# Optimization experiments

Hardware: AMD Instinct MI355X
Metric: run time of the kernel (lower is better)

The kernel has to match this reference:

```python
import jax, jax.numpy as jnp
import numpy as np
from jax import lax

COCO_80_TO_91 = [1,2,3,4,5,6,7,8,9,10,11,13,14,15,16,17,18,19,20,21,22,23,24,25,27,28,31,32,33,34,35,36,37,38,39,40,41,42,43,44,46,47,48,49,50,51,52,53,54,55,56,57,58,59,60,61,62,63,64,65,67,70,72,73,74,75,76,77,78,79,80,81,82,84,85,86,87,88,89,90]

CONF = 0.25      # self.confidence
IOU_THR = 0.7    # ultralytics NMS default
TOPK = 1000      # candidate cap before NMS
MAX_DET = 300    # ultralytics max_det default
MAX_WH = 7680.0  # per-class offset trick
IMG_SZ = 640.0   # yolov8 letterboxed input size


def setup_inputs() -> dict:
    key = jax.random.key(0)
    preds = jax.random.uniform(key, (32, 84, 8400), dtype=jnp.float32)
    return {"preds": preds}


def _nms_single(boxes, scores):
    """Greedy NMS on score-descending boxes [K,4] (class-offset xyxy). Returns keep mask [K]."""
    K = boxes.shape[0]
    area = (boxes[:, 2] - boxes[:, 0]) * (boxes[:, 3] - boxes[:, 1])  # [K]
    lt = jnp.maximum(boxes[:, None, :2], boxes[None, :, :2])          # [K,K,2]
    rb = jnp.minimum(boxes[:, None, 2:], boxes[None, :, 2:])
    wh = jnp.clip(rb - lt, 0.0)
    inter = wh[..., 0] * wh[..., 1]
    iou = inter / (area[:, None] + area[None, :] - inter + 1e-7)       # [K,K]
    idx = jnp.arange(K)
    sup = (iou > IOU_THR) & (idx[None, :] > idx[:, None])              # i suppresses later j

    def body(i, keep):
        return jnp.where(keep[i], keep & ~sup[i], keep)

    return lax.fori_loop(0, K, body, jnp.ones((K,), dtype=bool))


def reference(preds):
    # preds: [B, 84, N] -> [B, N, 84]
    p = jnp.transpose(preds, (0, 2, 1))
    box_xywh = p[..., :4] * IMG_SZ           # xywh in pixels on 640x640 canvas
    cls = p[..., 4:]                          # [B, N, 80]
    scores = jnp.max(cls, axis=-1)            # best-class confidence
    labels = jnp.argmax(cls, axis=-1)         # 0..79
    xy, wh = box_xywh[..., :2], box_xywh[..., 2:]
    xyxy = jnp.concatenate([xy - wh * 0.5, xy + wh * 0.5], axis=-1)  # decode

    # confidence filter + top-K candidate selection (score-descending)
    s_masked = jnp.where(scores > CONF, scores, -1.0)
    top_s, top_i = lax.top_k(s_masked, TOPK)                          # [B,TOPK]
    top_b = jnp.take_along_axis(xyxy, top_i[..., None], axis=1)      # [B,TOPK,4]
    top_l = jnp.take_along_axis(labels, top_i, axis=1)               # [B,TOPK]

    # per-class NMS via class offset
    off_b = top_b + (top_l.astype(top_b.dtype) * MAX_WH)[..., None]
    keep = jax.vmap(_nms_single)(off_b, top_s) & (top_s > CONF)

    # select final max_det detections, zero-pad invalid slots
    fin_s = jnp.where(keep, top_s, -1.0)
    out_s, out_i = lax.top_k(fin_s, MAX_DET)                          # [B,MAX_DET]
    out_b = jnp.take_along_axis(top_b, out_i[..., None], axis=1)
    out_l = jnp.take_along_axis(top_l, out_i, axis=1)
    valid = out_s > CONF
    boxes = jnp.where(valid[..., None], out_b, 0.0)
    scores_out = jnp.where(valid, out_s, 0.0)
    mapped = jnp.asarray(COCO_80_TO_91, dtype=jnp.int64)[out_l]       # COCO 80 -> 91 ids
    labels_out = jnp.where(valid, mapped, 0)
    return boxes, scores_out, labels_out
```

## Files before the change

### kernel.cpp

```cpp
#include <hip/hip_runtime.h>
#include <stdint.h>

typedef unsigned long long u64;
typedef unsigned int u32;

#define BATCH 32
#define NCH 84
#define NA 8400
#define NCLS 80
#define TOPK 1000
#define MAXDET 300
#define CONF 0.25f
#define IOU_T 0.7f
#define MAX_WH 7680.0f
#define IMG_SZ 640.0f
#define NT 1024
#define KPT 9
#define NCOPY 8
#define HPAD 260

__device__ __constant__ float coco_map_f[NCLS] = {
    1,2,3,4,5,6,7,8,9,10,11,13,14,15,16,17,18,19,20,21,22,23,24,25,27,28,
    31,32,33,34,35,36,37,38,39,40,41,42,43,44,46,47,48,49,50,51,52,53,54,
    55,56,57,58,59,60,61,62,63,64,65,67,70,72,73,74,75,76,77,78,79,80,81,
    82,84,85,86,87,88,89,90};

__device__ inline u64 shflx64(u64 v, int m) {
    int lo = __shfl_xor((int)(u32)(v & 0xFFFFFFFFull), m, 64);
    int hi = __shfl_xor((int)(u32)(v >> 32), m, 64);
    return ((u64)(u32)hi << 32) | (u32)lo;
}

__global__ __launch_bounds__(256)
void decode_kernel(const float* __restrict__ preds,
                   u64* __restrict__ keys,
                   float4* __restrict__ boxes,
                   int* __restrict__ labels) {
    const int QPB = NA / 4;
    int gid = blockIdx.x * 256 + threadIdx.x;
    if (gid >= BATCH * QPB) return;
    int b = gid / QPB;
    int q = gid - b * QPB;
    int a0 = q * 4;
    const float* p = preds + (size_t)b * NCH * NA + a0;

    float4 x = *(const float4*)(p);
    float4 y = *(const float4*)(p + NA);
    float4 w = *(const float4*)(p + 2 * NA);
    float4 h = *(const float4*)(p + 3 * NA);

    float4 best = *(const float4*)(p + 4 * NA);
    int lx = 0, ly = 0, lz = 0, lw = 0;
#pragma unroll 16
    for (int c = 1; c < NCLS; ++c) {
        const float4 v = *(const float4*)(p + (size_t)(4 + c) * NA);
        lx = (v.x > best.x) ? c : lx;  best.x = fmaxf(v.x, best.x);
        ly = (v.y > best.y) ? c : ly;  best.y = fmaxf(v.y, best.y);
        lz = (v.z > best.z) ? c : lz;  best.z = fmaxf(v.z, best.z);
        lw = (v.w > best.w) ? c : lw;  best.w = fmaxf(v.w, best.w);
    }

    float bs[4] = {best.x, best.y, best.z, best.w};
    int   bl[4] = {lx, ly, lz, lw};
    float cx[4] = {x.x, x.y, x.z, x.w};
    float cy[4] = {y.x, y.y, y.z, y.w};
    float cw[4] = {w.x, w.y, w.z, w.w};
    float ch[4] = {h.x, h.y, h.z, h.w};

    u64* kp = keys + (size_t)b * NA + a0;
    float4* bp = boxes + (size_t)b * NA + a0;
    int* lp = labels + (size_t)b * NA + a0;

#pragma unroll
    for (int i = 0; i < 4; ++i) {
        float fx = cx[i] * IMG_SZ, fy = cy[i] * IMG_SZ;
        float fw = cw[i] * IMG_SZ, fh = ch[i] * IMG_SZ;
        float hw = fw * 0.5f, hh = fh * 0.5f;
        bp[i] = make_float4(fx - hw, fy - hh, fx + hw, fy + hh);
        float s = (bs[i] > CONF) ? bs[i] : -1.0f;
        u32 fb = __float_as_uint(s);
        u32 u = (fb & 0x80000000u) ? ~fb : (fb | 0x80000000u);
        kp[i] = ((u64)u << 14) | (u64)(16383 - (a0 + i));
    }
    *(int4*)lp = make_int4(bl[0], bl[1], bl[2], bl[3]);
}

__global__ __launch_bounds__(NT)
void select_nms_kernel(const u64* __restrict__ keys,
                       const float4* __restrict__ boxes,
                       const int* __restrict__ labels,
                       float* __restrict__ out) {
    const int b = blockIdx.x;
    const int t = threadIdx.x;
    const int lane = t & 63, wid = t >> 6;

    __shared__ u64 skey[NT];
    __shared__ float offb[TOPK][4];
    __shared__ float area_s[TOPK];
    __shared__ unsigned char lb8[TOPK];
    __shared__ unsigned char keep[TOPK];
    __shared__ u64 cmask2[NCLS][16];
    __shared__ unsigned short rows[NCLS][64];
    __shared__ int sh_hist[NCOPY * HPAD];
    __shared__ int selB, selK, hselS, cnt, nselS, ktot_s;
    __shared__ int wsum[16], woff[16];

    u64 kreg[KPT];
    const u64* kb = keys + (size_t)b * NA;
    int nk = 0;
    for (int i = t; i < NA; i += NT) kreg[nk++] = kb[i];

    u64 P = 0ull;
    int kk = TOPK;
    int nsel = 0;
    for (int d = 5; d >= 0; --d) {
        for (int i = t; i < NCOPY * HPAD; i += NT) sh_hist[i] = 0;
        __syncthreads();
        u64 hmask = (~0ull) << (8 * (d + 1));
        int* myh = sh_hist + (wid & (NCOPY - 1)) * HPAD;
        for (int i = 0; i < KPT; ++i) {
            if (i < nk) {
                u64 key = kreg[i];
                if (((key ^ P) & hmask) == 0ull)
                    atomicAdd(&myh[(int)((key >> (8 * d)) & 255)], 1);
            }
        }
        __syncthreads();
        if (t < 64) {
            int h0 = 0, h1 = 0, h2 = 0, h3 = 0;
            for (int c = 0; c < NCOPY; ++c) {
                const int* hp = sh_hist + c * HPAD + 4 * t;
                h0 += hp[0]; h1 += hp[1]; h2 += hp[2]; h3 += hp[3];
            }
            int s = h0 + h1 + h2 + h3;
            int S = s;
            #pragma unroll
            for (int off = 1; off < 64; off <<= 1) {
                int o = __shfl_down(S, off, 64);
                if (t + off < 64) S += o;
            }
            int Snext = S - s;
            int c3 = Snext + h3, c2 = c3 + h2, c1 = c2 + h1, c0 = c1 + h0;
            int cand = -1, above = 0;
            if (c0 >= kk) {
                if      (c3 >= kk) { cand = 4 * t + 3; above = Snext; }
                else if (c2 >= kk) { cand = 4 * t + 2; above = c3; }
                else if (c1 >= kk) { cand = 4 * t + 1; above = c2; }
                else               { cand = 4 * t;     above = c1; }
            }
            int pc = (cand < 0) ? 0 : (((cand + 1) << 16) | (kk - above));
            #pragma unroll
            for (int off = 32; off; off >>= 1)
                pc = max(pc, __shfl_down(pc, off, 64));
            pc = __shfl(pc, 0, 64);
            int B = (pc >> 16) - 1;
            if (t == (B >> 2)) {
                int m4 = B & 3;
                selB = B;
                selK = pc & 0xFFFF;
                hselS = (m4 == 0) ? h0 : (m4 == 1) ? h1 : (m4 == 2) ? h2 : h3;
            }
        }
        __syncthreads();
        P |= ((u64)selB) << (8 * d);
        kk = selK;
        nsel = TOPK - kk + hselS;
        if (nsel <= NT) break;
        __syncthreads();
    }

    if (t == 0) cnt = 0;
    __syncthreads();
    for (int i = 0; i < KPT; ++i) {
        bool p = (i < nk) && (kreg[i] >= P);
        u64 m = __ballot(p);
        int base = 0;
        if (lane == 0) base = atomicAdd(&cnt, (int)__popcll(m));
        base = __shfl(base, 0, 64);
        if (p) skey[base + (int)__popcll(m & ((1ull << lane) - 1ull))] = kreg[i];
    }
    if (t < NT - nsel) skey[nsel + t] = 0ull;
    __syncthreads();

    u64 myk = skey[t];
    for (int size = 2; size <= NT; size <<= 1) {
        bool up = ((t & size) == 0);
        for (int stride = size >> 1; stride; stride >>= 1) {
            u64 pk;
            if (stride >= 64) {
                __syncthreads(); skey[t] = myk; __syncthreads();
                pk = skey[t ^ stride];
            } else {
                pk = shflx64(myk, stride);
            }
            bool tlow = ((t & stride) == 0);
            u64 mn = (myk < pk) ? myk : pk;
            u64 mx = (myk < pk) ? pk : myk;
            myk = up ? (tlow ? mx : mn) : (tlow ? mn : mx);
        }
    }

    for (int i = t; i < NCLS * 16; i += NT) ((u64*)cmask2)[i] = 0ull;
    __syncthreads();

    int my_a = -1, my_L = 0;
    if (t < TOPK) {
        my_a = 16383 - (int)(myk & 16383ull);
        my_L = labels[(size_t)b * NA + my_a];
        lb8[t] = (unsigned char)my_L;
        float4 bx = boxes[(size_t)b * NA + my_a];
        float off = (float)my_L * MAX_WH;
        float ox0 = bx.x + off, oy0 = bx.y + off, ox1 = bx.z + off, oy1 = bx.w + off;
        offb[t][0] = ox0; offb[t][1] = oy0; offb[t][2] = ox1; offb[t][3] = oy1;
        area_s[t] = (ox1 - ox0) * (oy1 - oy0);
        keep[t] = 1;
        atomicOr(&cmask2[my_L][t >> 6], 1ull << (t & 63));
    }
    __syncthreads();

    for (int c = wid; c < NCLS; c += 16) {
        u64 w = (lane < 16) ? cmask2[c][lane] : 0ull;
        int cw = __popcll(w);
        int pre = cw;
        #pragma unroll
        for (int off = 1; off < 16; off <<= 1) {
            int o = __shfl_up(pre, off, 64);
            if (lane >= off) pre += o;
        }
        int n = __shfl(pre, 15, 64);
        pre -= cw;
        if (n == 0) continue;
        if (n <= 64) {
            if (lane < 16) {
                u64 ww = w; int base = pre, boff = lane << 6;
                while (ww) {
                    int bit = __ffsll((long long)ww) - 1;
                    ww &= ww - 1;
                    rows[c][base++] = (unsigned short)(boff + bit);
                }
            }
            int j = (lane < n) ? (int)rows[c][lane] : (int)rows[c][0];
            float x0 = offb[j][0], y0 = offb[j][1];
            float x1 = offb[j][2], y1 = offb[j][3];
            float ar = area_s[j];
            u64 colm = 0ull;
            for (int i = 0; i < n; ++i) {
                float hx0 = __shfl(x0, i, 64);
                float hy0 = __shfl(y0, i, 64);
                float hx1 = __shfl(x1, i, 64);
                float hy1 = __shfl(y1, i, 64);
                float ha  = __shfl(ar, i, 64);
                float lx = fmaxf(hx0, x0), ly = fmaxf(hy0, y0);
                float rx = fminf(hx1, x1), ry = fminf(hy1, y1);
                float ww2 = fmaxf(rx - lx, 0.0f);
                float hh2 = fmaxf(ry - ly, 0.0f);
                float inter = ww2 * hh2;
                float denom = ha + ar;
                denom = denom - inter;
                denom = denom + 1e-7f;
                bool s = (lane > i) && (lane < n) && (inter / denom > IOU_T);
                colm |= ((u64)s) << i;
            }
            u64 alive = (n >= 64) ? ~0ull : ((1ull << n) - 1ull);
            for (int i = 0; i < n; ++i) {
                if (!((alive >> i) & 1ull)) continue;
                alive &= ~__ballot((colm >> i) & 1ull);
            }
            if (lane < n) keep[j] = (unsigned char)((alive >> lane) & 1ull);
        } else if (lane == 0) {
            for (int i = 0; i < TOPK; ++i) {
                if (lb8[i] != (unsigned char)c || !keep[i]) continue;
                float ax0 = offb[i][0], ay0 = offb[i][1];
                float ax1 = offb[i][2], ay1 = offb[i][3];
                float aa = area_s[i];
                for (int j2 = i + 1; j2 < TOPK; ++j2) {
                    if (lb8[j2] != (unsigned char)c || !keep[j2]) continue;
                    float lx = fmaxf(ax0, offb[j2][0]);
                    float ly = fmaxf(ay0, offb[j2][1]);
                    float rx = fminf(ax1, offb[j2][2]);
                    float ry = fminf(ay1, offb[j2][3]);
                    float ww2 = fmaxf(rx - lx, 0.0f);
                    float hh2 = fmaxf(ry - ly, 0.0f);
                    float inter = ww2 * hh2;
                    float denom = aa + area_s[j2];
                    denom = denom - inter;
                    denom = denom + 1e-7f;
                    if (inter / denom > IOU_T) keep[j2] = 0;
                }
            }
        }
    }
    __syncthreads();

    bool valid = false;
    float sj = 0.0f;
    if (t < TOPK) {
        u32 u = (u32)(myk >> 14);
        u32 fb = (u & 0x80000000u) ? (u ^ 0x80000000u) : ~u;
        sj = __uint_as_float(fb);
        valid = keep[t] && (sj > CONF);
    }
    u64 m = __ballot(valid);
    if (lane == 0) wsum[wid] = (int)__popcll(m);
    __syncthreads();
    if (wid == 0) {
        int v = (lane < 16) ? wsum[lane] : 0;
        #pragma unroll
        for (int off = 1; off < 16; off <<= 1) {
            int o = __shfl_up(v, off, 64);
            if (lane >= off) v += o;
        }
        if (lane < 16) woff[lane] = v - wsum[lane];
        if (lane == 15) ktot_s = v;
    }
    __syncthreads();
    int ktot = ktot_s;
    int rank = woff[wid] + (int)__popcll(m & ((1ull << lane) - 1ull));

    float* out_boxes = out;
    float* out_scores = out + (size_t)BATCH * MAXDET * 4;
    float* out_labels = out + (size_t)BATCH * MAXDET * 5;
    if (valid && rank < MAXDET) {
        float4 bx = boxes[(size_t)b * NA + my_a];
        float* ob = out_boxes + ((size_t)b * MAXDET + rank) * 4;
        ob[0] = bx.x; ob[1] = bx.y; ob[2] = bx.z; ob[3] = bx.w;
        out_scores[(size_t)b * MAXDET + rank] = sj;
        out_labels[(size_t)b * MAXDET + rank] = coco_map_f[my_L];
    }
    if (t < MAXDET && t >= ktot) {
        float* ob = out_boxes + ((size_t)b * MAXDET + t) * 4;
        ob[0] = 0.0f; ob[1] = 0.0f; ob[2] = 0.0f; ob[3] = 0.0f;
        out_scores[(size_t)b * MAXDET + t] = 0.0f;
        out_labels[(size_t)b * MAXDET + t] = 0.0f;
    }
}

extern "C" void kernel_launch(void* const* d_in, const int* in_sizes, int n_in,
                              void* d_out, int out_size, void* d_ws, size_t ws_size,
                              hipStream_t stream) {
    const float* preds = (const float*)d_in[0];
    char* ws = (char*)d_ws;

    const size_t keys_bytes = (size_t)BATCH * NA * 8;
    const size_t boxes_bytes = (size_t)BATCH * NA * 16;

    u64* keys = (u64*)ws;
    float4* boxes = (float4*)(ws + keys_bytes);
    int* labels = (int*)(ws + keys_bytes + boxes_bytes);
    float* out = (float*)d_out;

    int total = BATCH * (NA / 4);
    decode_kernel<<<(total + 255) / 256, 256, 0, stream>>>(preds, keys, boxes, labels);
    select_nms_kernel<<<BATCH, NT, 0, stream>>>(keys, boxes, labels, out);
}
```

Measured before the change: 193.2 us.

## Split select/NMS kernel, add max-bucket fast path and double-buffered bitonic sort

Splits the fused top-K selection and NMS kernel into a separate top-K/sort kernel and an NMS kernel, passing sorted keys through global memory. The radix select first checks whether the highest occupied digit bucket alone covers the remaining K, which skips the histogram pass when it does. The shared-memory stages of the bitonic sort use two alternating buffers, so each stage needs one barrier instead of two. The split adds one kernel launch and a global round-trip of the sorted keys.

```diff
diff --git a/kernel.cpp b/kernel.cpp
--- a/kernel.cpp
+++ b/kernel.cpp
@@ -86,24 +86,15 @@
 }
 
 __global__ __launch_bounds__(NT)
-void select_nms_kernel(const u64* __restrict__ keys,
-                       const float4* __restrict__ boxes,
-                       const int* __restrict__ labels,
-                       float* __restrict__ out) {
+void topk_sort_kernel(const u64* __restrict__ keys,
+                      u64* __restrict__ sorted) {
     const int b = blockIdx.x;
     const int t = threadIdx.x;
     const int lane = t & 63, wid = t >> 6;
 
-    __shared__ u64 skey[NT];
-    __shared__ float offb[TOPK][4];
-    __shared__ float area_s[TOPK];
-    __shared__ unsigned char lb8[TOPK];
-    __shared__ unsigned char keep[TOPK];
-    __shared__ u64 cmask2[NCLS][16];
-    __shared__ unsigned short rows[NCLS][64];
+    __shared__ u64 sk[2][NT];
     __shared__ int sh_hist[NCOPY * HPAD];
-    __shared__ int selB, selK, hselS, cnt, nselS, ktot_s;
-    __shared__ int wsum[16], woff[16];
+    __shared__ int selB, selK, hselS, smax, scnt, cnt;
 
     u64 kreg[KPT];
     const u64* kb = keys + (size_t)b * NA;
@@ -114,17 +105,44 @@
     int kk = TOPK;
     int nsel = 0;
     for (int d = 5; d >= 0; --d) {
+        __syncthreads();
+        if (t == 0) { smax = -1; scnt = 0; }
+        __syncthreads();
+        u64 hmask = (~0ull) << (8 * (d + 1));
+        int dig[KPT];
+        int mymax = -1;
+#pragma unroll
+        for (int i = 0; i < KPT; ++i) {
+            bool act = (i < nk) && (((kreg[i] ^ P) & hmask) == 0ull);
+            dig[i] = act ? (int)((kreg[i] >> (8 * d)) & 255) : -1;
+            mymax = max(mymax, dig[i]);
+        }
+#pragma unroll
+        for (int off = 32; off; off >>= 1)
+            mymax = max(mymax, __shfl_down(mymax, off, 64));
+        if (lane == 0) atomicMax(&smax, mymax);
+        __syncthreads();
+        int maxb = smax;
+        int myc = 0;
+#pragma unroll
+        for (int i = 0; i < KPT; ++i) myc += (dig[i] == maxb) ? 1 : 0;
+#pragma unroll
+        for (int off = 32; off; off >>= 1) myc += __shfl_down(myc, off, 64);
+        if (lane == 0) atomicAdd(&scnt, myc);
+        __syncthreads();
+        int cm = scnt;
+        if (cm >= kk) {
+            P |= ((u64)maxb) << (8 * d);
+            nsel = TOPK - kk + cm;
+            if (nsel <= NT) break;
+            continue;
+        }
         for (int i = t; i < NCOPY * HPAD; i += NT) sh_hist[i] = 0;
         __syncthreads();
-        u64 hmask = (~0ull) << (8 * (d + 1));
         int* myh = sh_hist + (wid & (NCOPY - 1)) * HPAD;
-        for (int i = 0; i < KPT; ++i) {
-            if (i < nk) {
-                u64 key = kreg[i];
-                if (((key ^ P) & hmask) == 0ull)
-                    atomicAdd(&myh[(int)((key >> (8 * d)) & 255)], 1);
-            }
-        }
+#pragma unroll
+        for (int i = 0; i < KPT; ++i)
+            if (dig[i] >= 0) atomicAdd(&myh[dig[i]], 1);
         __syncthreads();
         if (t < 64) {
             int h0 = 0, h1 = 0, h2 = 0, h3 = 0;
@@ -166,9 +184,9 @@
         kk = selK;
         nsel = TOPK - kk + hselS;
         if (nsel <= NT) break;
-        __syncthreads();
-    }
-
+    }
+
+    __syncthreads();
     if (t == 0) cnt = 0;
     __syncthreads();
     for (int i = 0; i < KPT; ++i) {
@@ -177,19 +195,22 @@
         int base = 0;
         if (lane == 0) base = atomicAdd(&cnt, (int)__popcll(m));
         base = __shfl(base, 0, 64);
-        if (p) skey[base + (int)__popcll(m & ((1ull << lane) - 1ull))] = kreg[i];
-    }
-    if (t < NT - nsel) skey[nsel + t] = 0ull;
-    __syncthreads();
-
-    u64 myk = skey[t];
+        if (p) sk[0][base + (int)__popcll(m & ((1ull << lane) - 1ull))] = kreg[i];
+    }
+    if (t < NT - nsel) sk[0][nsel + t] = 0ull;
+    __syncthreads();
+
+    u64 myk = sk[0][t];
+    int buf = 1;
     for (int size = 2; size <= NT; size <<= 1) {
         bool up = ((t & size) == 0);
         for (int stride = size >> 1; stride; stride >>= 1) {
             u64 pk;
             if (stride >= 64) {
-                __syncthreads(); skey[t] = myk; __syncthreads();
-                pk = skey[t ^ stride];
+                sk[buf][t] = myk;
+                __syncthreads();
+                pk = sk[buf][t ^ stride];
+                buf ^= 1;
             } else {
                 pk = shflx64(myk, stride);
             }
@@ -199,6 +220,28 @@
             myk = up ? (tlow ? mx : mn) : (tlow ? mn : mx);
         }
     }
+    sorted[(size_t)b * NT + t] = myk;
+}
+
+__global__ __launch_bounds__(NT)
+void nms_kernel(const u64* __restrict__ sorted,
+                const float4* __restrict__ boxes,
+                const int* __restrict__ labels,
+                float* __restrict__ out) {
+    const int b = blockIdx.x;
+    const int t = threadIdx.x;
+    const int lane = t & 63, wid = t >> 6;
+
+    __shared__ float offb[TOPK][4];
+    __shared__ float area_s[TOPK];
+    __shared__ unsigned char lb8[TOPK];
+    __shared__ unsigned char keep[TOPK];
+    __shared__ u64 cmask2[NCLS][16];
+    __shared__ unsigned short rows[NCLS][64];
+    __shared__ int ktot_s;
+    __shared__ int wsum[16], woff[16];
+
+    u64 myk = sorted[(size_t)b * NT + t];
 
     for (int i = t; i < NCLS * 16; i += NT) ((u64*)cmask2)[i] = 0ull;
     __syncthreads();
@@ -341,15 +384,18 @@
     const float* preds = (const float*)d_in[0];
     char* ws = (char*)d_ws;
 
-    const size_t keys_bytes = (size_t)BATCH * NA * 8;
-    const size_t boxes_bytes = (size_t)BATCH * NA * 16;
+    const size_t keys_bytes   = (size_t)BATCH * NA * 8;
+    const size_t boxes_bytes  = (size_t)BATCH * NA * 16;
+    const size_t labels_bytes = (size_t)BATCH * NA * 4;
 
     u64* keys = (u64*)ws;
     float4* boxes = (float4*)(ws + keys_bytes);
     int* labels = (int*)(ws + keys_bytes + boxes_bytes);
+    u64* sorted = (u64*)(ws + keys_bytes + boxes_bytes + labels_bytes);
     float* out = (float*)d_out;
 
     int total = BATCH * (NA / 4);
     decode_kernel<<<(total + 255) / 256, 256, 0, stream>>>(preds, keys, boxes, labels);
-    select_nms_kernel<<<BATCH, NT, 0, stream>>>(keys, boxes, labels, out);
+    topk_sort_kernel<<<BATCH, NT, 0, stream>>>(keys, sorted);
+    nms_kernel<<<BATCH, NT, 0, stream>>>(sorted, boxes, labels, out);
 }
```

Measured after the change: 187.8 us. 1.03x faster.
